# Kernel optimization log

Hardware: AMD Instinct MI355X
Metric: run time of the kernel (lower is better)

Reference implementation:

```python
import jax, jax.numpy as jnp
import numpy as np

N, D, H, G = 4096, 256, 4, 16
HEAD_DIM = D // H
LN_EPS = 1e-5
TEMP = 5.0


def setup_inputs() -> dict:
    key = jax.random.key(0)
    ks = jax.random.split(key, 12)
    s = 0.05  # weight init scale
    nrm = lambda k, shp: jax.random.normal(k, shp, jnp.float32) * s
    return {
        "x": jax.random.normal(ks[0], (N, D), jnp.float32),
        "Wq": nrm(ks[1], (D, D)), "bq": jnp.zeros((D,), jnp.float32),
        "Wk": nrm(ks[2], (D, D)), "bk": jnp.zeros((D,), jnp.float32),
        "Wv": nrm(ks[3], (D, D)), "bv": jnp.zeros((D,), jnp.float32),
        "Wv1": nrm(ks[4], (D, D // 2)), "bv1": jnp.zeros((D // 2,), jnp.float32),
        "Wv2": nrm(ks[5], (D // 2, 1)), "bv2": jnp.zeros((1,), jnp.float32),
        "Wc1": nrm(ks[6], (2 * D, D)), "bc1": jnp.zeros((D,), jnp.float32),
        "Wc2": nrm(ks[7], (D, 1)), "bc2": jnp.zeros((1,), jnp.float32),
        "gamma": jnp.ones((D,), jnp.float32),
        "beta": jnp.zeros((D,), jnp.float32),
        "batch": jnp.sort(jax.random.randint(ks[8], (N,), 0, G)),
    }


def reference(x, Wq, bq, Wk, bk, Wv, bv, Wv1, bv1, Wv2, bv2,
              Wc1, bc1, Wc2, bc2, gamma, beta, batch):
    n = x.shape[0]
    # multi-head projections -> [N, H, head_dim]
    Q = (x @ Wq + bq).reshape(n, H, HEAD_DIM)
    K = (x @ Wk + bk).reshape(n, H, HEAD_DIM)
    V = (x @ Wv + bv).reshape(n, H, HEAD_DIM)

    # dense scores [N, N, H], block-diagonal mask by graph membership
    scores = jnp.einsum('nhd,mhd->nmh', Q, K) / np.sqrt(HEAD_DIM).astype(np.float32)
    same_graph = (batch[:, None] == batch[None, :])  # [N, N]
    scores = jnp.where(same_graph[:, :, None], scores, -jnp.inf)
    probs = jax.nn.softmax(scores, axis=1)  # softmax over keys m (dim=1, as in torch)
    # dropout is identity in eval mode
    attended = jnp.einsum('nmh,mhd->nhd', probs, V).reshape(n, D)

    # vulnerability detector MLP: D -> D/2 -> 1, sigmoid
    vuln = jax.nn.sigmoid(jax.nn.relu(x @ Wv1 + bv1) @ Wv2 + bv2)[:, 0]

    # global max pool per graph, broadcast back to nodes
    graph_ctx = jax.ops.segment_max(x, batch, num_segments=G, indices_are_sorted=True)[batch]
    combined = jnp.concatenate([x, graph_ctx], axis=1)  # [N, 2D]
    ctx = jax.nn.sigmoid(jnp.tanh(combined @ Wc1 + bc1) @ Wc2 + bc2)[:, 0]

    mha_avg = probs.mean(axis=(1, 2))  # [N]
    w = 0.6 * vuln + 0.3 * ctx + 0.1 * mha_avg

    # per-graph segment softmax with temperature 5.0
    w5 = w * TEMP
    seg_max = jax.ops.segment_max(w5, batch, num_segments=G, indices_are_sorted=True)[batch]
    e = jnp.exp(w5 - seg_max)
    seg_sum = jax.ops.segment_sum(e, batch, num_segments=G, indices_are_sorted=True)[batch]
    att = e / seg_sum  # [N]

    out = attended * att[:, None] + x  # residual
    # LayerNorm over last dim
    mu = out.mean(axis=-1, keepdims=True)
    var = out.var(axis=-1, keepdims=True)
    out = (out - mu) * jax.lax.rsqrt(var + LN_EPS) * gamma + beta
    return out, att
```

## Files before the change

### kernel.cpp

```cpp
#include <hip/hip_runtime.h>
#include <math.h>

#define N_NODES 4096
#define DIM 256
#define NH 4
#define NG 16
#define LN_EPS 1e-5f
#define TEMP 5.0f
#define RSLACK 4160
#define PS_STRIDE 72
#define BS_STRIDE 264
#define QT_MAX 24
#define KC_MAX 6
#define WPG (KC_MAX * QT_MAX * NH)
#define ATTN_UNITS (NG * WPG / 4)

typedef __attribute__((ext_vector_type(8))) short short8;
typedef __attribute__((ext_vector_type(4))) short short4_t;
typedef __attribute__((ext_vector_type(4))) float f32x4;

__device__ __forceinline__ unsigned short f2bf(float f) {
    unsigned u = __builtin_bit_cast(unsigned, f);
    u += 0x7FFFu + ((u >> 16) & 1u);
    return (unsigned short)(u >> 16);
}
__device__ __forceinline__ float bf2f(unsigned short u) {
    return __builtin_bit_cast(float, (unsigned)u << 16);
}
__device__ __forceinline__ float fsigmoid(float z) { return 1.f / (1.f + __expf(-z)); }
__device__ __forceinline__ float ftanh(float z) {
    float t = __expf(2.f * z);
    return (t - 1.f) / (t + 1.f);
}
__device__ __forceinline__ int seg_search(const int* __restrict__ batch, int g) {
    int lo = 0, hi = N_NODES;
    while (lo < hi) {
        int mid = (lo + hi) >> 1;
        if (batch[mid] < g) lo = mid + 1; else hi = mid;
    }
    return lo;
}

__device__ __forceinline__ short8 afrag_f32(const float* __restrict__ x, int row, int k0) {
    float4 a = *(const float4*)&x[(size_t)row * 256 + k0];
    float4 b = *(const float4*)&x[(size_t)row * 256 + k0 + 4];
    short8 r = {(short)f2bf(a.x), (short)f2bf(a.y), (short)f2bf(a.z), (short)f2bf(a.w),
                (short)f2bf(b.x), (short)f2bf(b.y), (short)f2bf(b.z), (short)f2bf(b.w)};
    return r;
}

__device__ __forceinline__ void ldsB(const float* __restrict__ W, int ws, int bn,
                                     int ncols, unsigned short* __restrict__ Bs) {
    int tpr = ncols >> 2;
    int c4 = (threadIdx.x & (tpr - 1)) * 4;
    int r0 = threadIdx.x / tpr;
    int rpp = 256 / tpr;
    for (int p = 0; p < (ncols >> 2); ++p) {
        int k = p * rpp + r0;
        float4 wv = *(const float4*)&W[(size_t)k * ws + bn + c4];
        Bs[(c4 + 0) * BS_STRIDE + k] = f2bf(wv.x);
        Bs[(c4 + 1) * BS_STRIDE + k] = f2bf(wv.y);
        Bs[(c4 + 2) * BS_STRIDE + k] = f2bf(wv.z);
        Bs[(c4 + 3) * BS_STRIDE + k] = f2bf(wv.w);
    }
    __syncthreads();
}

__global__ __launch_bounds__(256) void k1_kernel(
    const float* __restrict__ x,
    const float* __restrict__ Wq, const float* __restrict__ bq,
    const float* __restrict__ Wk, const float* __restrict__ bk,
    const float* __restrict__ Wv, const float* __restrict__ bv,
    const float* __restrict__ Wv1, const float* __restrict__ bv1,
    const float* __restrict__ Wv2, const float* __restrict__ Wc1,
    const int* __restrict__ batch,
    unsigned short* __restrict__ Qb, unsigned short* __restrict__ Kb,
    unsigned short* __restrict__ Vt, float* __restrict__ vacc2,
    float* __restrict__ gcw, int* __restrict__ seg) {
    __shared__ __align__(16) char smem[64 * BS_STRIDE * 2];
    int id = blockIdx.x, tid = threadIdx.x;
    if (id < 16) {
        int g = id;
        int s = seg_search(batch, g), e = seg_search(batch, g + 1);
        float* red = (float*)smem;
        float* gl  = (float*)smem + 1024;
        int c4 = (tid & 63) * 4, way = tid >> 6;
        float4 mx = {-INFINITY, -INFINITY, -INFINITY, -INFINITY};
        for (int i = s + way; i < e; i += 4) {
            float4 v = *(const float4*)&x[(size_t)i * DIM + c4];
            mx.x = fmaxf(mx.x, v.x); mx.y = fmaxf(mx.y, v.y);
            mx.z = fmaxf(mx.z, v.z); mx.w = fmaxf(mx.w, v.w);
        }
        *(float4*)&red[way * 256 + c4] = mx;
        __syncthreads();
        if (way == 0) {
#pragma unroll
            for (int j = 0; j < 4; ++j) {
                float mm = fmaxf(fmaxf(red[c4 + j], red[256 + c4 + j]),
                                 fmaxf(red[512 + c4 + j], red[768 + c4 + j]));
                gl[c4 + j] = bf2f(f2bf(mm));
            }
        }
        __syncthreads();
        float a0 = 0.f, a1 = 0.f, a2 = 0.f, a3 = 0.f;
        for (int k = 0; k < 256; k += 4) {
            a0 += gl[k + 0] * Wc1[(size_t)(256 + k + 0) * 256 + tid];
            a1 += gl[k + 1] * Wc1[(size_t)(256 + k + 1) * 256 + tid];
            a2 += gl[k + 2] * Wc1[(size_t)(256 + k + 2) * 256 + tid];
            a3 += gl[k + 3] * Wc1[(size_t)(256 + k + 3) * 256 + tid];
        }
        gcw[g * 256 + tid] = (a0 + a1) + (a2 + a3);
        return;
    }
    if (id == 16) {
        if (tid <= NG) seg[tid] = seg_search(batch, tid);
        return;
    }
    int u = id - 17;
    unsigned short* Bs = (unsigned short*)smem;
    int w = tid >> 6, lane = tid & 63, m = lane & 15, quad = lane >> 4;
    if (u < 768) {
        int z = u >> 8, r = u & 255, bx = r & 63, by = r >> 6;
        const float* W = (z == 0) ? Wq : (z == 1) ? Wk : Wv;
        const float* bias = (z == 0) ? bq : (z == 1) ? bk : bv;
        ldsB(W, 256, by * 64, 64, Bs);
        int rowA = bx * 64 + 16 * w + m;
        short8 a[8];
#pragma unroll
        for (int ks = 0; ks < 8; ++ks) a[ks] = afrag_f32(x, rowA, ks * 32 + quad * 8);
        int node0 = bx * 64 + 16 * w + quad * 4;
#pragma unroll
        for (int nt = 0; nt < 4; ++nt) {
            f32x4 acc = {0.f, 0.f, 0.f, 0.f};
#pragma unroll
            for (int ks = 0; ks < 8; ++ks) {
                short8 b = *(const short8*)&Bs[(nt * 16 + m) * BS_STRIDE + ks * 32 + quad * 8];
                acc = __builtin_amdgcn_mfma_f32_16x16x32_bf16(a[ks], b, acc, 0, 0, 0);
            }
            int col = by * 64 + nt * 16 + m;
            float bb = bias[col];
            if (z == 0) {
#pragma unroll
                for (int r2 = 0; r2 < 4; ++r2)
                    Qb[(size_t)(node0 + r2) * 256 + col] = f2bf((acc[r2] + bb) * 0.125f);
            } else if (z == 1) {
#pragma unroll
                for (int r2 = 0; r2 < 4; ++r2)
                    Kb[(size_t)(node0 + r2) * 256 + col] = f2bf(acc[r2] + bb);
            } else {
                short4_t pk = {(short)f2bf(acc[0] + bb), (short)f2bf(acc[1] + bb),
                               (short)f2bf(acc[2] + bb), (short)f2bf(acc[3] + bb)};
                *(short4_t*)&Vt[(size_t)col * RSLACK + node0] = pk;
            }
        }
    } else {
        int r = u - 768, bx = r & 63, by = r >> 6;
        ldsB(Wv1, 128, by * 64, 64, Bs);
        int rowA = bx * 64 + 16 * w + m;
        short8 a[8];
#pragma unroll
        for (int ks = 0; ks < 8; ++ks) a[ks] = afrag_f32(x, rowA, ks * 32 + quad * 8);
        int node0 = bx * 64 + 16 * w + quad * 4;
        float psum[4] = {0.f, 0.f, 0.f, 0.f};
#pragma unroll
        for (int nt = 0; nt < 4; ++nt) {
            f32x4 acc = {0.f, 0.f, 0.f, 0.f};
#pragma unroll
            for (int ks = 0; ks < 8; ++ks) {
                short8 b = *(const short8*)&Bs[(nt * 16 + m) * BS_STRIDE + ks * 32 + quad * 8];
                acc = __builtin_amdgcn_mfma_f32_16x16x32_bf16(a[ks], b, acc, 0, 0, 0);
            }
            int col = by * 64 + nt * 16 + m;
            float bb = bv1[col], wv = Wv2[col];
#pragma unroll
            for (int r2 = 0; r2 < 4; ++r2) psum[r2] += fmaxf(acc[r2] + bb, 0.f) * wv;
        }
#pragma unroll
        for (int r2 = 0; r2 < 4; ++r2) {
#pragma unroll
            for (int mm = 1; mm < 16; mm <<= 1) psum[r2] += __shfl_xor(psum[r2], mm);
            if (m == 0) vacc2[(size_t)(node0 + r2) * 2 + by] = psum[r2];
        }
    }
}

__global__ __launch_bounds__(256) void k2_kernel(
    const float* __restrict__ x, const float* __restrict__ Wc1,
    const float* __restrict__ bc1, const float* __restrict__ Wc2,
    const float* __restrict__ gcw, const int* __restrict__ batch,
    const unsigned short* __restrict__ Qb, const unsigned short* __restrict__ Kb,
    const unsigned short* __restrict__ Vt, const int* __restrict__ seg,
    unsigned short* __restrict__ Opart, float* __restrict__ Lpart,
    float* __restrict__ cacc16) {
    __shared__ __align__(16) char smem[9216];
    int tid = threadIdx.x;
    int w = tid >> 6, lane = tid & 63, m = lane & 15, quad = lane >> 4;
    if (blockIdx.x < 1024) {
        int bx = blockIdx.x & 63, by = blockIdx.x >> 6;
        unsigned short* Bs = (unsigned short*)smem;
        ldsB(Wc1, 256, by * 16, 16, Bs);
        int rowA = bx * 64 + 16 * w + m;
        short8 a[8];
#pragma unroll
        for (int ks = 0; ks < 8; ++ks) a[ks] = afrag_f32(x, rowA, ks * 32 + quad * 8);
        int node0 = bx * 64 + 16 * w + quad * 4;
        int b4[4];
#pragma unroll
        for (int r2 = 0; r2 < 4; ++r2) b4[r2] = batch[node0 + r2];
        f32x4 acc = {0.f, 0.f, 0.f, 0.f};
#pragma unroll
        for (int ks = 0; ks < 8; ++ks) {
            short8 b = *(const short8*)&Bs[m * BS_STRIDE + ks * 32 + quad * 8];
            acc = __builtin_amdgcn_mfma_f32_16x16x32_bf16(a[ks], b, acc, 0, 0, 0);
        }
        int col = by * 16 + m;
        float bb = bc1[col], wc = Wc2[col];
#pragma unroll
        for (int r2 = 0; r2 < 4; ++r2) {
            float p = ftanh(acc[r2] + bb + gcw[b4[r2] * 256 + col]) * wc;
#pragma unroll
            for (int mm = 1; mm < 16; mm <<= 1) p += __shfl_xor(p, mm);
            if (m == 0) cacc16[(size_t)(node0 + r2) * 16 + by] = p;
        }
        return;
    }
    unsigned short* Ps = (unsigned short*)smem;
    int wid = (blockIdx.x - 1024) * 4 + w;
    int g = wid / WPG;
    int r1 = wid - g * WPG;
    int kc = r1 / (QT_MAX * NH);
    int r2i = r1 - kc * (QT_MAX * NH);
    int qt = r2i >> 2, h = r2i & 3;
    int s = seg[g], e = seg[g + 1];
    int q0 = s + qt * 16;
    int k0 = s + kc * 64;
    if (q0 >= e || k0 >= e) return;

    short8 qa0 = *(const short8*)&Qb[(size_t)(q0 + m) * 256 + h * 64 + quad * 8];
    short8 qa1 = *(const short8*)&Qb[(size_t)(q0 + m) * 256 + h * 64 + 32 + quad * 8];

    f32x4 S[4];
#pragma unroll
    for (int nt = 0; nt < 4; ++nt) {
        int key = k0 + nt * 16 + m;
        short8 kb0 = *(const short8*)&Kb[(size_t)key * 256 + h * 64 + quad * 8];
        short8 kb1 = *(const short8*)&Kb[(size_t)key * 256 + h * 64 + 32 + quad * 8];
        f32x4 sa = {0.f, 0.f, 0.f, 0.f};
        sa = __builtin_amdgcn_mfma_f32_16x16x32_bf16(qa0, kb0, sa, 0, 0, 0);
        sa = __builtin_amdgcn_mfma_f32_16x16x32_bf16(qa1, kb1, sa, 0, 0, 0);
        S[nt] = sa;
    }
    int wbase = w * 16 * PS_STRIDE;
#pragma unroll
    for (int nt = 0; nt < 4; ++nt) {
        bool valid = (k0 + nt * 16 + m) < e;
#pragma unroll
        for (int r3 = 0; r3 < 4; ++r3) {
            float p = valid ? __expf(S[nt][r3]) : 0.f;
            Ps[wbase + (quad * 4 + r3) * PS_STRIDE + nt * 16 + m] = f2bf(p);
        }
    }
    __builtin_amdgcn_wave_barrier();
    short8 pa0 = *(const short8*)&Ps[wbase + m * PS_STRIDE + quad * 8];
    short8 pa1 = *(const short8*)&Ps[wbase + m * PS_STRIDE + 32 + quad * 8];

    short8 ones = {16256, 16256, 16256, 16256, 16256, 16256, 16256, 16256};
    f32x4 Lacc = {0.f, 0.f, 0.f, 0.f};
    Lacc = __builtin_amdgcn_mfma_f32_16x16x32_bf16(pa0, ones, Lacc, 0, 0, 0);
    Lacc = __builtin_amdgcn_mfma_f32_16x16x32_bf16(pa1, ones, Lacc, 0, 0, 0);
    f32x4 O[4];
#pragma unroll
    for (int nt = 0; nt < 4; ++nt) {
        const unsigned short* vrow = &Vt[(size_t)(h * 64 + nt * 16 + m) * RSLACK + k0];
        short8 vb0 = *(const short8*)&vrow[quad * 8];
        short8 vb1 = *(const short8*)&vrow[32 + quad * 8];
        f32x4 oa = {0.f, 0.f, 0.f, 0.f};
        oa = __builtin_amdgcn_mfma_f32_16x16x32_bf16(pa0, vb0, oa, 0, 0, 0);
        oa = __builtin_amdgcn_mfma_f32_16x16x32_bf16(pa1, vb1, oa, 0, 0, 0);
        O[nt] = oa;
    }
#pragma unroll
    for (int r3 = 0; r3 < 4; ++r3) {
        int q = q0 + quad * 4 + r3;
        if (q < e) {
            if (m == 0) Lpart[((size_t)kc * N_NODES + q) * 4 + h] = Lacc[r3];
#pragma unroll
            for (int nt = 0; nt < 4; ++nt)
                Opart[((size_t)kc * N_NODES + q) * 256 + h * 64 + nt * 16 + m] =
                    f2bf(O[nt][r3]);
        }
    }
}

__global__ __launch_bounds__(256) void k3_kernel(
    const unsigned short* __restrict__ Opart, const float* __restrict__ Lpart,
    const float* __restrict__ x, const float* __restrict__ vacc2,
    const float* __restrict__ cacc16, const float* __restrict__ bv2,
    const float* __restrict__ bc2, const float* __restrict__ gamma,
    const float* __restrict__ beta, const int* __restrict__ batch,
    const int* __restrict__ seg, float* __restrict__ out,
    float* __restrict__ att_out) {
    __shared__ float wsc[776];
    __shared__ float gm[8], gsum[8];
    __shared__ float r1[4], r2[4];
    int tid = threadIdx.x;
    int n0 = blockIdx.x * 8;
    int gf = batch[n0], gl = batch[n0 + 7];
    int s0 = seg[gf], e1 = seg[gl + 1];
    float vb = bv2[0], cb = bc2[0];
    for (int j = s0 + tid; j < e1; j += 256) {
        float2 vv = *(const float2*)&vacc2[(size_t)j * 2];
        float4 c0 = *(const float4*)&cacc16[(size_t)j * 16];
        float4 c1 = *(const float4*)&cacc16[(size_t)j * 16 + 4];
        float4 c2 = *(const float4*)&cacc16[(size_t)j * 16 + 8];
        float4 c3 = *(const float4*)&cacc16[(size_t)j * 16 + 12];
        float cs = ((c0.x + c0.y) + (c0.z + c0.w)) + ((c1.x + c1.y) + (c1.z + c1.w)) +
                   ((c2.x + c2.y) + (c2.z + c2.w)) + ((c3.x + c3.y) + (c3.z + c3.w));
        wsc[j - s0] = TEMP * (0.6f * fsigmoid(vv.x + vv.y + vb) +
                              0.3f * fsigmoid(cs + cb) + 0.1f / 4096.f);
    }
    __syncthreads();
    for (int g = gf; g <= gl; ++g) {
        int gs_ = seg[g], ge = seg[g + 1];
        float mx = -1e30f;
        for (int j = gs_ + tid; j < ge; j += 256) mx = fmaxf(mx, wsc[j - s0]);
#pragma unroll
        for (int k2 = 32; k2; k2 >>= 1) mx = fmaxf(mx, __shfl_xor(mx, k2));
        if ((tid & 63) == 0) r1[tid >> 6] = mx;
        __syncthreads();
        mx = fmaxf(fmaxf(r1[0], r1[1]), fmaxf(r1[2], r1[3]));
        float sm = 0.f;
        for (int j = gs_ + tid; j < ge; j += 256) sm += __expf(wsc[j - s0] - mx);
#pragma unroll
        for (int k2 = 32; k2; k2 >>= 1) sm += __shfl_xor(sm, k2);
        __syncthreads();
        if ((tid & 63) == 0) r2[tid >> 6] = sm;
        __syncthreads();
        if (tid == 0) {
            gm[g - gf] = mx;
            gsum[g - gf] = r2[0] + r2[1] + r2[2] + r2[3];
        }
        __syncthreads();
    }
    for (int i = 0; i < 8; ++i) {
        int n = n0 + i;
        int g = batch[n];
        int s = seg[g], e = seg[g + 1];
        float att_n = __expf(wsc[n - s0] - gm[g - gf]) / gsum[g - gf];
        if (tid == 0) att_out[n] = att_n;
        int h = tid >> 6;
        float L = 0.f, O = 0.f;
#pragma unroll
        for (int c = 0; c < KC_MAX; ++c) {
            bool valid = (s + c * 64) < e;
            float lv = Lpart[((size_t)c * N_NODES + n) * 4 + h];
            float ov = bf2f(Opart[((size_t)c * N_NODES + n) * 256 + tid]);
            if (valid) { L += lv; O += ov; }
        }
        float o = (O / L) * att_n + x[(size_t)n * 256 + tid];
        float s1 = o, s2 = o * o;
#pragma unroll
        for (int k2 = 32; k2; k2 >>= 1) {
            s1 += __shfl_xor(s1, k2);
            s2 += __shfl_xor(s2, k2);
        }
        __syncthreads();
        if ((tid & 63) == 0) { r1[tid >> 6] = s1; r2[tid >> 6] = s2; }
        __syncthreads();
        float mu = (r1[0] + r1[1] + r1[2] + r1[3]) * (1.f / 256.f);
        float ms = (r2[0] + r2[1] + r2[2] + r2[3]) * (1.f / 256.f);
        float rs = rsqrtf(ms - mu * mu + LN_EPS);
        out[(size_t)n * 256 + tid] = (o - mu) * rs * gamma[tid] + beta[tid];
    }
}

extern "C" void kernel_launch(void* const* d_in, const int* in_sizes, int n_in,
                              void* d_out, int out_size, void* d_ws, size_t ws_size,
                              hipStream_t stream) {
    const float* x     = (const float*)d_in[0];
    const float* Wq    = (const float*)d_in[1];
    const float* bq    = (const float*)d_in[2];
    const float* Wk    = (const float*)d_in[3];
    const float* bk    = (const float*)d_in[4];
    const float* Wv    = (const float*)d_in[5];
    const float* bv    = (const float*)d_in[6];
    const float* Wv1   = (const float*)d_in[7];
    const float* bv1   = (const float*)d_in[8];
    const float* Wv2   = (const float*)d_in[9];
    const float* bv2   = (const float*)d_in[10];
    const float* Wc1   = (const float*)d_in[11];
    const float* bc1   = (const float*)d_in[12];
    const float* Wc2   = (const float*)d_in[13];
    const float* bc2   = (const float*)d_in[14];
    const float* gamma = (const float*)d_in[15];
    const float* beta  = (const float*)d_in[16];
    const int*   batch = (const int*)d_in[17];

    float* out = (float*)d_out;
    float* att = out + N_NODES * DIM;

    float* vacc2  = (float*)d_ws;
    float* cacc16 = vacc2 + N_NODES * 2;
    float* gcw    = cacc16 + N_NODES * 16;
    float* Lpart  = gcw + NG * DIM;
    int*   seg    = (int*)(Lpart + KC_MAX * N_NODES * 4);
    unsigned short* Qb    = (unsigned short*)(seg + 32);
    unsigned short* Kb    = Qb + RSLACK * DIM;
    unsigned short* Vt    = Kb + RSLACK * DIM;
    unsigned short* Opart = Vt + DIM * RSLACK;

    k1_kernel<<<913, 256, 0, stream>>>(x, Wq, bq, Wk, bk, Wv, bv, Wv1, bv1, Wv2,
                                       Wc1, batch, Qb, Kb, Vt, vacc2, gcw, seg);
    k2_kernel<<<1024 + ATTN_UNITS, 256, 0, stream>>>(x, Wc1, bc1, Wc2, gcw, batch,
                                                     Qb, Kb, Vt, seg,
                                                     Opart, Lpart, cacc16);
    k3_kernel<<<N_NODES / 8, 256, 0, stream>>>(Opart, Lpart, x, vacc2, cacc16,
                                               bv2, bc2, gamma, beta, batch, seg,
                                               out, att);
}
```

Measured before the change: 174.1 us.

## Loop over key chunks inside attention waves and move context GEMM into k1

Each attention wave now walks every 64-key chunk of its graph and accumulates O and L in registers, so it writes one final output instead of one partial per chunk. k3 therefore reads a single O/L pair per node and skips the partial reduction. The x@Wc1 projection moves into k1 as a full 256-column bf16 MFMA GEMM that stores a pre-activation buffer, and k2 applies tanh plus the graph-context term per node. This cuts partial-result traffic and the per-16-column recompute of x fragments, at the cost of fewer, longer attention waves and a new fp32 N×D buffer to write and read.

Result: slower. 178.0 us (+2.2%).

```diff
diff --git a/kernel.cpp b/kernel.cpp
--- a/kernel.cpp
+++ b/kernel.cpp
@@ -11,9 +11,7 @@
 #define PS_STRIDE 72
 #define BS_STRIDE 264
 #define QT_MAX 24
-#define KC_MAX 6
-#define WPG (KC_MAX * QT_MAX * NH)
-#define ATTN_UNITS (NG * WPG / 4)
+#define ATTN_BLOCKS (NG * QT_MAX)
 
 typedef __attribute__((ext_vector_type(8))) short short8;
 typedef __attribute__((ext_vector_type(4))) short short4_t;
@@ -50,13 +48,11 @@
 }
 
 __device__ __forceinline__ void ldsB(const float* __restrict__ W, int ws, int bn,
-                                     int ncols, unsigned short* __restrict__ Bs) {
-    int tpr = ncols >> 2;
-    int c4 = (threadIdx.x & (tpr - 1)) * 4;
-    int r0 = threadIdx.x / tpr;
-    int rpp = 256 / tpr;
-    for (int p = 0; p < (ncols >> 2); ++p) {
-        int k = p * rpp + r0;
+                                     unsigned short* __restrict__ Bs) {
+    int c4 = (threadIdx.x & 15) * 4;
+    int r0 = threadIdx.x >> 4;
+    for (int p = 0; p < 16; ++p) {
+        int k = p * 16 + r0;
         float4 wv = *(const float4*)&W[(size_t)k * ws + bn + c4];
         Bs[(c4 + 0) * BS_STRIDE + k] = f2bf(wv.x);
         Bs[(c4 + 1) * BS_STRIDE + k] = f2bf(wv.y);
@@ -73,10 +69,10 @@
     const float* __restrict__ Wv, const float* __restrict__ bv,
     const float* __restrict__ Wv1, const float* __restrict__ bv1,
     const float* __restrict__ Wv2, const float* __restrict__ Wc1,
-    const int* __restrict__ batch,
+    const float* __restrict__ bc1, const int* __restrict__ batch,
     unsigned short* __restrict__ Qb, unsigned short* __restrict__ Kb,
     unsigned short* __restrict__ Vt, float* __restrict__ vacc2,
-    float* __restrict__ gcw, int* __restrict__ seg) {
+    float* __restrict__ Tpre, float* __restrict__ gcw, int* __restrict__ seg) {
     __shared__ __align__(16) char smem[64 * BS_STRIDE * 2];
     int id = blockIdx.x, tid = threadIdx.x;
     if (id < 16) {
@@ -123,7 +119,7 @@
         int z = u >> 8, r = u & 255, bx = r & 63, by = r >> 6;
         const float* W = (z == 0) ? Wq : (z == 1) ? Wk : Wv;
         const float* bias = (z == 0) ? bq : (z == 1) ? bk : bv;
-        ldsB(W, 256, by * 64, 64, Bs);
+        ldsB(W, 256, by * 64, Bs);
         int rowA = bx * 64 + 16 * w + m;
         short8 a[8];
 #pragma unroll
@@ -153,9 +149,9 @@
                 *(short4_t*)&Vt[(size_t)col * RSLACK + node0] = pk;
             }
         }
-    } else {
+    } else if (u < 896) {
         int r = u - 768, bx = r & 63, by = r >> 6;
-        ldsB(Wv1, 128, by * 64, 64, Bs);
+        ldsB(Wv1, 128, by * 64, Bs);
         int rowA = bx * 64 + 16 * w + m;
         short8 a[8];
 #pragma unroll
@@ -181,121 +177,124 @@
             for (int mm = 1; mm < 16; mm <<= 1) psum[r2] += __shfl_xor(psum[r2], mm);
             if (m == 0) vacc2[(size_t)(node0 + r2) * 2 + by] = psum[r2];
         }
+    } else {
+        int r = u - 896, bx = r & 63, by = r >> 6;
+        ldsB(Wc1, 256, by * 64, Bs);
+        int rowA = bx * 64 + 16 * w + m;
+        short8 a[8];
+#pragma unroll
+        for (int ks = 0; ks < 8; ++ks) a[ks] = afrag_f32(x, rowA, ks * 32 + quad * 8);
+        int node0 = bx * 64 + 16 * w + quad * 4;
+#pragma unroll
+        for (int nt = 0; nt < 4; ++nt) {
+            f32x4 acc = {0.f, 0.f, 0.f, 0.f};
+#pragma unroll
+            for (int ks = 0; ks < 8; ++ks) {
+                short8 b = *(const short8*)&Bs[(nt * 16 + m) * BS_STRIDE + ks * 32 + quad * 8];
+                acc = __builtin_amdgcn_mfma_f32_16x16x32_bf16(a[ks], b, acc, 0, 0, 0);
+            }
+            int col = by * 64 + nt * 16 + m;
+            float bb = bc1[col];
+#pragma unroll
+            for (int r2 = 0; r2 < 4; ++r2)
+                Tpre[(size_t)(node0 + r2) * 256 + col] = acc[r2] + bb;
+        }
     }
 }
 
 __global__ __launch_bounds__(256) void k2_kernel(
-    const float* __restrict__ x, const float* __restrict__ Wc1,
-    const float* __restrict__ bc1, const float* __restrict__ Wc2,
-    const float* __restrict__ gcw, const int* __restrict__ batch,
+    const float* __restrict__ Tpre, const float* __restrict__ gcw,
+    const float* __restrict__ Wc2, const int* __restrict__ batch,
     const unsigned short* __restrict__ Qb, const unsigned short* __restrict__ Kb,
     const unsigned short* __restrict__ Vt, const int* __restrict__ seg,
-    unsigned short* __restrict__ Opart, float* __restrict__ Lpart,
-    float* __restrict__ cacc16) {
-    __shared__ __align__(16) char smem[9216];
+    unsigned short* __restrict__ Ofin, float* __restrict__ Lfin,
+    float* __restrict__ cacc) {
+    __shared__ __align__(16) unsigned short Ps[4 * 16 * PS_STRIDE];
     int tid = threadIdx.x;
+    if (blockIdx.x < 256) {
+        int nl = tid >> 4, cs = (tid & 15) * 16;
+        int node = blockIdx.x * 16 + nl;
+        int g = batch[node];
+        float sum = 0.f;
+#pragma unroll
+        for (int j = 0; j < 16; ++j) {
+            int c = cs + j;
+            sum += ftanh(Tpre[(size_t)node * 256 + c] + gcw[g * 256 + c]) * Wc2[c];
+        }
+#pragma unroll
+        for (int mm = 1; mm < 16; mm <<= 1) sum += __shfl_xor(sum, mm);
+        if ((tid & 15) == 0) cacc[node] = sum;
+        return;
+    }
+    int b = blockIdx.x - 256;
+    int g = b / QT_MAX, qt = b - g * QT_MAX;
     int w = tid >> 6, lane = tid & 63, m = lane & 15, quad = lane >> 4;
-    if (blockIdx.x < 1024) {
-        int bx = blockIdx.x & 63, by = blockIdx.x >> 6;
-        unsigned short* Bs = (unsigned short*)smem;
-        ldsB(Wc1, 256, by * 16, 16, Bs);
-        int rowA = bx * 64 + 16 * w + m;
-        short8 a[8];
-#pragma unroll
-        for (int ks = 0; ks < 8; ++ks) a[ks] = afrag_f32(x, rowA, ks * 32 + quad * 8);
-        int node0 = bx * 64 + 16 * w + quad * 4;
-        int b4[4];
-#pragma unroll
-        for (int r2 = 0; r2 < 4; ++r2) b4[r2] = batch[node0 + r2];
-        f32x4 acc = {0.f, 0.f, 0.f, 0.f};
-#pragma unroll
-        for (int ks = 0; ks < 8; ++ks) {
-            short8 b = *(const short8*)&Bs[m * BS_STRIDE + ks * 32 + quad * 8];
-            acc = __builtin_amdgcn_mfma_f32_16x16x32_bf16(a[ks], b, acc, 0, 0, 0);
-        }
-        int col = by * 16 + m;
-        float bb = bc1[col], wc = Wc2[col];
-#pragma unroll
-        for (int r2 = 0; r2 < 4; ++r2) {
-            float p = ftanh(acc[r2] + bb + gcw[b4[r2] * 256 + col]) * wc;
-#pragma unroll
-            for (int mm = 1; mm < 16; mm <<= 1) p += __shfl_xor(p, mm);
-            if (m == 0) cacc16[(size_t)(node0 + r2) * 16 + by] = p;
-        }
-        return;
-    }
-    unsigned short* Ps = (unsigned short*)smem;
-    int wid = (blockIdx.x - 1024) * 4 + w;
-    int g = wid / WPG;
-    int r1 = wid - g * WPG;
-    int kc = r1 / (QT_MAX * NH);
-    int r2i = r1 - kc * (QT_MAX * NH);
-    int qt = r2i >> 2, h = r2i & 3;
+    int h = w;
     int s = seg[g], e = seg[g + 1];
     int q0 = s + qt * 16;
-    int k0 = s + kc * 64;
-    if (q0 >= e || k0 >= e) return;
+    if (q0 >= e) return;
 
     short8 qa0 = *(const short8*)&Qb[(size_t)(q0 + m) * 256 + h * 64 + quad * 8];
     short8 qa1 = *(const short8*)&Qb[(size_t)(q0 + m) * 256 + h * 64 + 32 + quad * 8];
-
-    f32x4 S[4];
-#pragma unroll
-    for (int nt = 0; nt < 4; ++nt) {
-        int key = k0 + nt * 16 + m;
-        short8 kb0 = *(const short8*)&Kb[(size_t)key * 256 + h * 64 + quad * 8];
-        short8 kb1 = *(const short8*)&Kb[(size_t)key * 256 + h * 64 + 32 + quad * 8];
-        f32x4 sa = {0.f, 0.f, 0.f, 0.f};
-        sa = __builtin_amdgcn_mfma_f32_16x16x32_bf16(qa0, kb0, sa, 0, 0, 0);
-        sa = __builtin_amdgcn_mfma_f32_16x16x32_bf16(qa1, kb1, sa, 0, 0, 0);
-        S[nt] = sa;
-    }
+    short8 ones = {16256, 16256, 16256, 16256, 16256, 16256, 16256, 16256};
+    f32x4 O[4];
+    f32x4 Lacc = {0.f, 0.f, 0.f, 0.f};
+#pragma unroll
+    for (int nt = 0; nt < 4; ++nt) O[nt] = (f32x4){0.f, 0.f, 0.f, 0.f};
     int wbase = w * 16 * PS_STRIDE;
-#pragma unroll
-    for (int nt = 0; nt < 4; ++nt) {
-        bool valid = (k0 + nt * 16 + m) < e;
-#pragma unroll
-        for (int r3 = 0; r3 < 4; ++r3) {
-            float p = valid ? __expf(S[nt][r3]) : 0.f;
-            Ps[wbase + (quad * 4 + r3) * PS_STRIDE + nt * 16 + m] = f2bf(p);
-        }
-    }
-    __builtin_amdgcn_wave_barrier();
-    short8 pa0 = *(const short8*)&Ps[wbase + m * PS_STRIDE + quad * 8];
-    short8 pa1 = *(const short8*)&Ps[wbase + m * PS_STRIDE + 32 + quad * 8];
-
-    short8 ones = {16256, 16256, 16256, 16256, 16256, 16256, 16256, 16256};
-    f32x4 Lacc = {0.f, 0.f, 0.f, 0.f};
-    Lacc = __builtin_amdgcn_mfma_f32_16x16x32_bf16(pa0, ones, Lacc, 0, 0, 0);
-    Lacc = __builtin_amdgcn_mfma_f32_16x16x32_bf16(pa1, ones, Lacc, 0, 0, 0);
-    f32x4 O[4];
-#pragma unroll
-    for (int nt = 0; nt < 4; ++nt) {
-        const unsigned short* vrow = &Vt[(size_t)(h * 64 + nt * 16 + m) * RSLACK + k0];
-        short8 vb0 = *(const short8*)&vrow[quad * 8];
-        short8 vb1 = *(const short8*)&vrow[32 + quad * 8];
-        f32x4 oa = {0.f, 0.f, 0.f, 0.f};
-        oa = __builtin_amdgcn_mfma_f32_16x16x32_bf16(pa0, vb0, oa, 0, 0, 0);
-        oa = __builtin_amdgcn_mfma_f32_16x16x32_bf16(pa1, vb1, oa, 0, 0, 0);
-        O[nt] = oa;
+
+    for (int k0 = s; k0 < e; k0 += 64) {
+        f32x4 S[4];
+#pragma unroll
+        for (int nt = 0; nt < 4; ++nt) {
+            int key = k0 + nt * 16 + m;
+            short8 kb0 = *(const short8*)&Kb[(size_t)key * 256 + h * 64 + quad * 8];
+            short8 kb1 = *(const short8*)&Kb[(size_t)key * 256 + h * 64 + 32 + quad * 8];
+            f32x4 sa = {0.f, 0.f, 0.f, 0.f};
+            sa = __builtin_amdgcn_mfma_f32_16x16x32_bf16(qa0, kb0, sa, 0, 0, 0);
+            sa = __builtin_amdgcn_mfma_f32_16x16x32_bf16(qa1, kb1, sa, 0, 0, 0);
+            S[nt] = sa;
+        }
+        __builtin_amdgcn_wave_barrier();
+#pragma unroll
+        for (int nt = 0; nt < 4; ++nt) {
+            bool valid = (k0 + nt * 16 + m) < e;
+#pragma unroll
+            for (int r3 = 0; r3 < 4; ++r3) {
+                float p = valid ? __expf(S[nt][r3]) : 0.f;
+                Ps[wbase + (quad * 4 + r3) * PS_STRIDE + nt * 16 + m] = f2bf(p);
+            }
+        }
+        __builtin_amdgcn_wave_barrier();
+        short8 pa0 = *(const short8*)&Ps[wbase + m * PS_STRIDE + quad * 8];
+        short8 pa1 = *(const short8*)&Ps[wbase + m * PS_STRIDE + 32 + quad * 8];
+        Lacc = __builtin_amdgcn_mfma_f32_16x16x32_bf16(pa0, ones, Lacc, 0, 0, 0);
+        Lacc = __builtin_amdgcn_mfma_f32_16x16x32_bf16(pa1, ones, Lacc, 0, 0, 0);
+#pragma unroll
+        for (int nt = 0; nt < 4; ++nt) {
+            const unsigned short* vrow = &Vt[(size_t)(h * 64 + nt * 16 + m) * RSLACK + k0];
+            short8 vb0 = *(const short8*)&vrow[quad * 8];
+            short8 vb1 = *(const short8*)&vrow[32 + quad * 8];
+            O[nt] = __builtin_amdgcn_mfma_f32_16x16x32_bf16(pa0, vb0, O[nt], 0, 0, 0);
+            O[nt] = __builtin_amdgcn_mfma_f32_16x16x32_bf16(pa1, vb1, O[nt], 0, 0, 0);
+        }
     }
 #pragma unroll
     for (int r3 = 0; r3 < 4; ++r3) {
         int q = q0 + quad * 4 + r3;
         if (q < e) {
-            if (m == 0) Lpart[((size_t)kc * N_NODES + q) * 4 + h] = Lacc[r3];
+            if (m == 0) Lfin[(size_t)q * 4 + h] = Lacc[r3];
 #pragma unroll
             for (int nt = 0; nt < 4; ++nt)
-                Opart[((size_t)kc * N_NODES + q) * 256 + h * 64 + nt * 16 + m] =
-                    f2bf(O[nt][r3]);
+                Ofin[(size_t)q * 256 + h * 64 + nt * 16 + m] = f2bf(O[nt][r3]);
         }
     }
 }
 
 __global__ __launch_bounds__(256) void k3_kernel(
-    const unsigned short* __restrict__ Opart, const float* __restrict__ Lpart,
+    const unsigned short* __restrict__ Ofin, const float* __restrict__ Lfin,
     const float* __restrict__ x, const float* __restrict__ vacc2,
-    const float* __restrict__ cacc16, const float* __restrict__ bv2,
+    const float* __restrict__ cacc, const float* __restrict__ bv2,
     const float* __restrict__ bc2, const float* __restrict__ gamma,
     const float* __restrict__ beta, const int* __restrict__ batch,
     const int* __restrict__ seg, float* __restrict__ out,
@@ -310,14 +309,8 @@
     float vb = bv2[0], cb = bc2[0];
     for (int j = s0 + tid; j < e1; j += 256) {
         float2 vv = *(const float2*)&vacc2[(size_t)j * 2];
-        float4 c0 = *(const float4*)&cacc16[(size_t)j * 16];
-        float4 c1 = *(const float4*)&cacc16[(size_t)j * 16 + 4];
-        float4 c2 = *(const float4*)&cacc16[(size_t)j * 16 + 8];
-        float4 c3 = *(const float4*)&cacc16[(size_t)j * 16 + 12];
-        float cs = ((c0.x + c0.y) + (c0.z + c0.w)) + ((c1.x + c1.y) + (c1.z + c1.w)) +
-                   ((c2.x + c2.y) + (c2.z + c2.w)) + ((c3.x + c3.y) + (c3.z + c3.w));
         wsc[j - s0] = TEMP * (0.6f * fsigmoid(vv.x + vv.y + vb) +
-                              0.3f * fsigmoid(cs + cb) + 0.1f / 4096.f);
+                              0.3f * fsigmoid(cacc[j] + cb) + 0.1f / 4096.f);
     }
     __syncthreads();
     for (int g = gf; g <= gl; ++g) {
@@ -342,21 +335,14 @@
         }
         __syncthreads();
     }
+    int h = tid >> 6;
     for (int i = 0; i < 8; ++i) {
         int n = n0 + i;
         int g = batch[n];
-        int s = seg[g], e = seg[g + 1];
         float att_n = __expf(wsc[n - s0] - gm[g - gf]) / gsum[g - gf];
         if (tid == 0) att_out[n] = att_n;
-        int h = tid >> 6;
-        float L = 0.f, O = 0.f;
-#pragma unroll
-        for (int c = 0; c < KC_MAX; ++c) {
-            bool valid = (s + c * 64) < e;
-            float lv = Lpart[((size_t)c * N_NODES + n) * 4 + h];
-            float ov = bf2f(Opart[((size_t)c * N_NODES + n) * 256 + tid]);
-            if (valid) { L += lv; O += ov; }
-        }
+        float L = Lfin[(size_t)n * 4 + h];
+        float O = bf2f(Ofin[(size_t)n * 256 + tid]);
         float o = (O / L) * att_n + x[(size_t)n * 256 + tid];
         float s1 = o, s2 = o * o;
 #pragma unroll
@@ -399,22 +385,24 @@
     float* out = (float*)d_out;
     float* att = out + N_NODES * DIM;
 
-    float* vacc2  = (float*)d_ws;
-    float* cacc16 = vacc2 + N_NODES * 2;
-    float* gcw    = cacc16 + N_NODES * 16;
-    float* Lpart  = gcw + NG * DIM;
-    int*   seg    = (int*)(Lpart + KC_MAX * N_NODES * 4);
-    unsigned short* Qb    = (unsigned short*)(seg + 32);
-    unsigned short* Kb    = Qb + RSLACK * DIM;
-    unsigned short* Vt    = Kb + RSLACK * DIM;
-    unsigned short* Opart = Vt + DIM * RSLACK;
-
-    k1_kernel<<<913, 256, 0, stream>>>(x, Wq, bq, Wk, bk, Wv, bv, Wv1, bv1, Wv2,
-                                       Wc1, batch, Qb, Kb, Vt, vacc2, gcw, seg);
-    k2_kernel<<<1024 + ATTN_UNITS, 256, 0, stream>>>(x, Wc1, bc1, Wc2, gcw, batch,
+    float* vacc2 = (float*)d_ws;
+    float* cacc  = vacc2 + N_NODES * 2;
+    float* gcw   = cacc + N_NODES;
+    float* Lfin  = gcw + NG * DIM;
+    float* Tpre  = Lfin + N_NODES * 4;
+    int*   seg   = (int*)(Tpre + N_NODES * DIM);
+    unsigned short* Qb   = (unsigned short*)(seg + 32);
+    unsigned short* Kb   = Qb + RSLACK * DIM;
+    unsigned short* Vt   = Kb + RSLACK * DIM;
+    unsigned short* Ofin = Vt + DIM * RSLACK;
+
+    k1_kernel<<<1169, 256, 0, stream>>>(x, Wq, bq, Wk, bk, Wv, bv, Wv1, bv1, Wv2,
+                                        Wc1, bc1, batch, Qb, Kb, Vt, vacc2, Tpre,
+                                        gcw, seg);
+    k2_kernel<<<256 + ATTN_BLOCKS, 256, 0, stream>>>(Tpre, gcw, Wc2, batch,
                                                      Qb, Kb, Vt, seg,
-                                                     Opart, Lpart, cacc16);
-    k3_kernel<<<N_NODES / 8, 256, 0, stream>>>(Opart, Lpart, x, vacc2, cacc16,
+                                                     Ofin, Lfin, cacc);
+    k3_kernel<<<N_NODES / 8, 256, 0, stream>>>(Ofin, Lfin, x, vacc2, cacc,
                                                bv2, bc2, gamma, beta, batch, seg,
                                                out, att);
 }
```
